# Performance work log

Hardware: AMD Instinct MI355X
Metric: run time of the kernel (lower is better)

Reference implementation:

```python
import jax, jax.numpy as jnp
import numpy as np

N_NODES = 50000

def _add_self_loops(edge_index, n):
    loop = jnp.arange(n, dtype=edge_index.dtype)
    src = jnp.concatenate([edge_index[0], loop])
    dst = jnp.concatenate([edge_index[1], loop])
    return src, dst

def _gcn_conv(x, src, dst, W, b, n):
    h = x @ W
    deg = jax.ops.segment_sum(jnp.ones_like(dst, dtype=h.dtype), dst, num_segments=n)
    inv_sqrt = jnp.where(deg > 0, jax.lax.rsqrt(deg), 0.0)
    coef = inv_sqrt[src] * inv_sqrt[dst]            # [E]
    msg = h[src] * coef[:, None]                     # [E, hidden]
    return jax.ops.segment_sum(msg, dst, num_segments=n) + b

def _gat_conv(x, src, dst, W, att_src, att_dst, b, n, heads, out_dim):
    # PyG GATConv, concat=False -> mean over heads; self-loops already added
    h = (x @ W).reshape(n, heads, out_dim)           # [N, H, F]
    a_src = jnp.sum(h * att_src, axis=-1)            # [N, H]
    a_dst = jnp.sum(h * att_dst, axis=-1)            # [N, H]
    e = a_src[src] + a_dst[dst]                      # [E, H]
    e = jax.nn.leaky_relu(e, negative_slope=0.2)
    # neighborhood softmax over edges grouped by destination
    m = jax.ops.segment_max(e, dst, num_segments=n)  # [N, H]
    ex = jnp.exp(e - m[dst])
    denom = jax.ops.segment_sum(ex, dst, num_segments=n)
    alpha = ex / denom[dst]                          # [E, H]
    out = jax.ops.segment_sum(h[src] * alpha[:, :, None], dst, num_segments=n)  # [N, H, F]
    return out.mean(axis=1) + b                      # concat=False -> head mean

def setup_inputs() -> dict:
    key = jax.random.key(0)
    ks = jax.random.split(key, 12)
    n, input_dim, hidden, output_dim, heads = N_NODES, 128, 128, 64, 2
    gat_out = hidden // 2
    x = jax.random.normal(ks[0], (n, input_dim), dtype=jnp.float32)
    edge_index = jax.random.randint(ks[1], (2, 800000), 0, n, dtype=jnp.int64)
    s = lambda fi, fo: float(np.sqrt(1.0 / fi))
    W1 = jax.random.normal(ks[2], (input_dim, hidden), dtype=jnp.float32) * s(input_dim, hidden)
    b1 = jnp.zeros((hidden,), dtype=jnp.float32)
    Wg = jax.random.normal(ks[3], (hidden, heads * gat_out), dtype=jnp.float32) * s(hidden, gat_out)
    att_src = jax.random.normal(ks[4], (heads, gat_out), dtype=jnp.float32) * s(gat_out, 1)
    att_dst = jax.random.normal(ks[5], (heads, gat_out), dtype=jnp.float32) * s(gat_out, 1)
    bg = jnp.zeros((gat_out,), dtype=jnp.float32)
    W3 = jax.random.normal(ks[6], (gat_out, output_dim), dtype=jnp.float32) * s(gat_out, output_dim)
    b3 = jnp.zeros((output_dim,), dtype=jnp.float32)
    return {"x": x, "edge_index": edge_index, "W1": W1, "b1": b1, "Wg": Wg,
            "att_src": att_src, "att_dst": att_dst, "bg": bg, "W3": W3, "b3": b3}

def reference(x, edge_index, W1, b1, Wg, att_src, att_dst, bg, W3, b3):
    n = x.shape[0]
    heads, gat_out = att_src.shape
    src, dst = _add_self_loops(edge_index, n)
    # dropout is identity in eval mode
    h = _gcn_conv(x, src, dst, W1, b1, n)
    h = jax.nn.relu(h)
    h = _gat_conv(h, src, dst, Wg, att_src, att_dst, bg, n, heads, gat_out)
    h = jax.nn.elu(h)
    return _gcn_conv(h, src, dst, W3, b3, n)
```

## Files before the change

kernel.cpp:

```cpp
#include <hip/hip_runtime.h>
#include <hip/hip_bf16.h>
#include <math.h>

#define N_NODES 50000
#define E0      800000
#define E_TOT   (E0 + N_NODES)
#define SCAP    512

using bf16 = __hip_bfloat16;
typedef __attribute__((ext_vector_type(8))) short bfrag;
typedef __attribute__((ext_vector_type(4))) float ffrag;

static __device__ __forceinline__ float bfu2f_lo(unsigned u){ return __uint_as_float(u << 16); }
static __device__ __forceinline__ float bfu2f_hi(unsigned u){ return __uint_as_float(u & 0xffff0000u); }

static __device__ __forceinline__ unsigned packbf(float a, float b){
    bf16 x = __float2bfloat16(a), y = __float2bfloat16(b);
    unsigned short ux = *reinterpret_cast<unsigned short*>(&x);
    unsigned short uy = *reinterpret_cast<unsigned short*>(&y);
    return ((unsigned)uy << 16) | ux;
}

static __device__ __forceinline__ int detect_f32(const unsigned* xu){
    int lane = threadIdx.x & 63;
    unsigned ex = (xu[lane] >> 7) & 0xFF;
    return (__ballot(ex < 100 || ex > 140) != 0ULL);
}
static __device__ __forceinline__ int detect_i32(const int* ei){
    int lane = threadIdx.x & 63;
    return (__ballot(ei[2 * lane + 1] != 0) != 0ULL);
}

static __device__ __forceinline__ float ldany(const void* p, int i, int isf32){
    return isf32 ? ((const float*)p)[i] : __bfloat162float(((const bf16*)p)[i]);
}

__global__ void k_convert(const void* __restrict__ xv,
                          const void* W1, const void* Wg, const void* W3,
                          const void* b1, const void* bg, const void* b3,
                          const void* as_, const void* ad_,
                          bf16* __restrict__ W1p, bf16* __restrict__ Wgp,
                          bf16* __restrict__ W3p, float* __restrict__ vecf,
                          bf16* __restrict__ xb, int* __restrict__ deg){
    const int NXB = (N_NODES * 32 + 255) / 256;
    int b = blockIdx.x, t = threadIdx.x;
    if (b >= 148 + NXB){
        int i = (b - 148 - NXB) * 256 + t;
        if (i < N_NODES) deg[i] = 0;
        return;
    }
    int isf = detect_f32((const unsigned*)xv);
    if (b >= 148){
        int i = (b - 148) * 256 + t;
        if (i < N_NODES * 32){
            if (isf){
                float4 v = ((const float4*)xv)[i];
                ((uint2*)xb)[i] = make_uint2(packbf(v.x, v.y), packbf(v.z, v.w));
            } else {
                ((uint2*)xb)[i] = ((const uint2*)xv)[i];
            }
        }
        return;
    }
    if (b < 16){
        int dd = b * 256 + t;
        int j  = dd & 7;
        int L  = (dd >> 3) & 63;
        int kc = (dd >> 9) & 1;
        int ct = dd >> 10;
        int k = kc * 32 + ((L >> 4) << 3) + j;
        int n = ct * 16 + (L & 15);
        W3p[dd] = __float2bfloat16(ldany(W3, k * 64 + n, isf));
    }
    else if (b < 18){
        int i = (b - 16) * 256 + t;
        float v;
        if      (i < 128) v = ldany(b1,  i,       isf);
        else if (i < 192) v = ldany(bg,  i - 128, isf);
        else if (i < 256) v = ldany(b3,  i - 192, isf);
        else if (i < 384) v = ldany(as_, i - 256, isf);
        else              v = ldany(ad_, i - 384, isf);
        vecf[i] = v;
    } else {
        int d = (b - 18) * 256 + t;
        const void* Wsrc = (d < 16384) ? W1 : Wg;
        bf16* Wdst = (d < 16384) ? W1p : Wgp;
        int dd = d & 16383;
        int j  = dd & 7;
        int L  = (dd >> 3) & 63;
        int kc = (dd >> 9) & 3;
        int ct = dd >> 11;
        int k = kc * 32 + ((L >> 4) << 3) + j;
        int n = ct * 16 + (L & 15);
        Wdst[dd] = __float2bfloat16(ldany(Wsrc, k * 128 + n, isf));
    }
}


static __device__ __forceinline__ int load_dst(const int* ei, int e, int is32){
    if (e >= E0) return e - E0;
    return is32 ? ei[E0 + e] : (int)((const long long*)ei)[E0 + e];
}
static __device__ __forceinline__ int load_src(const int* ei, int e, int is32){
    if (e >= E0) return e - E0;
    return is32 ? ei[e] : (int)((const long long*)ei)[e];
}

__global__ void k_count(const int* __restrict__ ei, int* __restrict__ deg,
                        int* __restrict__ rank){
    int is32 = detect_i32(ei);
    int e = blockIdx.x * blockDim.x + threadIdx.x;
    if (e >= E_TOT) return;
    int dst = load_dst(ei, e, is32);
    int src = load_src(ei, e, is32);
    if ((unsigned)dst >= N_NODES || (unsigned)src >= N_NODES) return;
    rank[e] = atomicAdd(&deg[dst], 1);
}

__global__ void k_scanA(const int* __restrict__ deg, int* __restrict__ tmp, int* __restrict__ blk){
    __shared__ int s[256];
    int t = threadIdx.x;
    int i = blockIdx.x * 256 + t;
    int v = (i < N_NODES) ? deg[i] : 0;
    s[t] = v; __syncthreads();
    for (int off = 1; off < 256; off <<= 1){
        int x = (t >= off) ? s[t - off] : 0;
        __syncthreads();
        s[t] += x;
        __syncthreads();
    }
    if (t == 255) blk[blockIdx.x] = s[255];
    if (i < N_NODES) tmp[i] = s[t] - v;
}

__global__ void k_scanC(int* __restrict__ row_ptr, const int* __restrict__ blk,
                        const int* __restrict__ deg, float* __restrict__ inv_sqrt,
                        int nb){
    __shared__ int s[256];
    int t = threadIdx.x;
    int B = blockIdx.x;
    s[t] = (t < nb && t < B) ? blk[t] : 0;
    __syncthreads();
    for (int off = 128; off; off >>= 1){
        if (t < off) s[t] += s[t + off];
        __syncthreads();
    }
    int base = s[0];
    int i = B * 256 + t;
    if (i < N_NODES){
        row_ptr[i] += base;
        int d = deg[i];
        inv_sqrt[i] = (d > 0) ? rsqrtf((float)d) : 0.0f;
    }
    if (i == 0) row_ptr[N_NODES] = E_TOT;
}

__global__ void k_fill(const int* __restrict__ ei, const int* __restrict__ row_ptr,
                       const float* __restrict__ isq, const int* __restrict__ rank,
                       int2* __restrict__ ecr){
    int is32 = detect_i32(ei);
    int e = blockIdx.x * blockDim.x + threadIdx.x;
    if (e >= E_TOT) return;
    int dst = load_dst(ei, e, is32);
    int src = load_src(ei, e, is32);
    if ((unsigned)dst >= N_NODES || (unsigned)src >= N_NODES) return;
    int pos = row_ptr[dst] + rank[e];
    float c = isq[dst] * isq[src];
    ecr[pos] = make_int2(src, __float_as_int(c));
}

__global__ __launch_bounds__(256) void k_gather(
        const uint4* __restrict__ xb16, const int* __restrict__ rp,
        const int2* __restrict__ ecr, uint4* __restrict__ Xa16){
    __shared__ int   scsr[SCAP];
    __shared__ float scf[SCAP];
    int n0 = blockIdx.x * 4;
    int b0 = rp[n0];
    int stot = min(rp[n0 + 4] - b0, SCAP);
    for (int i = threadIdx.x; i < stot; i += 256){
        int2 ev = ecr[b0 + i];
        scsr[i] = ev.x;
        scf[i]  = __int_as_float(ev.y);
    }
    __syncthreads();

    int w = threadIdx.x >> 6, lane = threadIdx.x & 63;
    int q4 = lane >> 4, fz = lane & 15;
    int n = n0 + w;
    float a0=0,a1=0,a2=0,a3=0,a4=0,a5=0,a6=0,a7=0;
    int b = rp[n] - b0, e = rp[n + 1] - b0;
    int elim = min(e, stot);
    #pragma unroll 2
    for (int i = b + q4; i < elim; i += 4){
        int s = scsr[i];
        float c = scf[i];
        uint4 v = xb16[(size_t)s * 16 + fz];
        a0 += c * bfu2f_lo(v.x);  a1 += c * bfu2f_hi(v.x);
        a2 += c * bfu2f_lo(v.y);  a3 += c * bfu2f_hi(v.y);
        a4 += c * bfu2f_lo(v.z);  a5 += c * bfu2f_hi(v.z);
        a6 += c * bfu2f_lo(v.w);  a7 += c * bfu2f_hi(v.w);
    }
    int start = max(b, stot);
    int i0 = start + (((b + q4) - start) & 3);
    for (int i = i0; i < e; i += 4){
        int2 ev = ecr[b0 + i];
        float c = __int_as_float(ev.y);
        uint4 v = xb16[(size_t)ev.x * 16 + fz];
        a0 += c * bfu2f_lo(v.x);  a1 += c * bfu2f_hi(v.x);
        a2 += c * bfu2f_lo(v.y);  a3 += c * bfu2f_hi(v.y);
        a4 += c * bfu2f_lo(v.z);  a5 += c * bfu2f_hi(v.z);
        a6 += c * bfu2f_lo(v.w);  a7 += c * bfu2f_hi(v.w);
    }
    a0 += __shfl_xor(a0, 32, 64);  a0 += __shfl_xor(a0, 16, 64);
    a1 += __shfl_xor(a1, 32, 64);  a1 += __shfl_xor(a1, 16, 64);
    a2 += __shfl_xor(a2, 32, 64);  a2 += __shfl_xor(a2, 16, 64);
    a3 += __shfl_xor(a3, 32, 64);  a3 += __shfl_xor(a3, 16, 64);
    a4 += __shfl_xor(a4, 32, 64);  a4 += __shfl_xor(a4, 16, 64);
    a5 += __shfl_xor(a5, 32, 64);  a5 += __shfl_xor(a5, 16, 64);
    a6 += __shfl_xor(a6, 32, 64);  a6 += __shfl_xor(a6, 16, 64);
    a7 += __shfl_xor(a7, 32, 64);  a7 += __shfl_xor(a7, 16, 64);
    if (lane < 16){
        uint4 o;
        o.x = packbf(a0, a1);  o.y = packbf(a2, a3);
        o.z = packbf(a4, a5);  o.w = packbf(a6, a7);
        Xa16[(size_t)n * 16 + fz] = o;
    }
}

template<int EPI>
__global__ __launch_bounds__(512) void k_gemm_mfma(
        const bf16* __restrict__ A, const bf16* __restrict__ Wp,
        const float* __restrict__ vecf, bf16* __restrict__ O,
        float* __restrict__ aS, float* __restrict__ aD){
    __shared__ float sA[16][8];
    __shared__ float sD[16][8];
    int wid  = threadIdx.x >> 6;
    int lane = threadIdx.x & 63;
    int n0 = blockIdx.x * 16;
    int m = lane & 15, q = lane >> 4;

    const bfrag* Ap = (const bfrag*)(A + (size_t)(n0 + m) * 128);
    const bfrag* Bp = (const bfrag*)Wp + (size_t)wid * 256 + lane;

    ffrag c = {0.f, 0.f, 0.f, 0.f};
    #pragma unroll
    for (int kc = 0; kc < 4; ++kc){
        bfrag af = Ap[kc * 4 + q];
        bfrag bf = Bp[kc * 64];
        c = __builtin_amdgcn_mfma_f32_16x16x32_bf16(af, bf, c, 0, 0, 0);
    }
    __syncthreads();

    int col = wid * 16 + m;
    if (EPI == 0){
        float bb = vecf[col];
        #pragma unroll
        for (int r = 0; r < 4; ++r){
            int row = n0 + q * 4 + r;
            O[(size_t)row * 128 + col] = __float2bfloat16(fmaxf(c[r] + bb, 0.f));
        }
    } else {
        int f = col & 63, h = col >> 6;
        float as_v = vecf[256 + h * 64 + f];
        float ad_v = vecf[384 + h * 64 + f];
        float ps[4], pd[4];
        #pragma unroll
        for (int r = 0; r < 4; ++r){
            int row = n0 + q * 4 + r;
            O[(size_t)row * 128 + f * 2 + h] = __float2bfloat16(c[r]);
            ps[r] = c[r] * as_v;
            pd[r] = c[r] * ad_v;
        }
        #pragma unroll
        for (int off = 1; off < 16; off <<= 1){
            #pragma unroll
            for (int r = 0; r < 4; ++r){
                ps[r] += __shfl_xor(ps[r], off, 64);
                pd[r] += __shfl_xor(pd[r], off, 64);
            }
        }
        if (m == 0){
            #pragma unroll
            for (int r = 0; r < 4; ++r){
                int rl = q * 4 + r;
                sA[rl][wid] = ps[r];
                sD[rl][wid] = pd[r];
            }
        }
        __syncthreads();
        int t = threadIdx.x;
        if (t < 64){
            int rl = t >> 2, hh = (t >> 1) & 1, which = t & 1;
            const float (*S)[8] = which ? sD : sA;
            float v = S[rl][hh * 4 + 0] + S[rl][hh * 4 + 1]
                    + S[rl][hh * 4 + 2] + S[rl][hh * 4 + 3];
            float* dp = which ? aD : aS;
            dp[(size_t)(n0 + rl) * 2 + hh] = v;
        }
    }
}

__global__ __launch_bounds__(256) void k_gemm_z(
        const bf16* __restrict__ Y, const bf16* __restrict__ W3p,
        bf16* __restrict__ Z){
    int wid  = threadIdx.x >> 6;
    int lane = threadIdx.x & 63;
    int n0 = blockIdx.x * 16;
    int m = lane & 15, q = lane >> 4;

    const bfrag* Ap = (const bfrag*)(Y + (size_t)(n0 + m) * 64);
    const bfrag* Bp = (const bfrag*)W3p + (size_t)wid * 128 + lane;

    ffrag c = {0.f, 0.f, 0.f, 0.f};
    #pragma unroll
    for (int kc = 0; kc < 2; ++kc){
        bfrag af = Ap[kc * 4 + q];
        bfrag bf = Bp[kc * 64];
        c = __builtin_amdgcn_mfma_f32_16x16x32_bf16(af, bf, c, 0, 0, 0);
    }
    int col = wid * 16 + m;
    #pragma unroll
    for (int r = 0; r < 4; ++r){
        int row = n0 + q * 4 + r;
        Z[(size_t)row * 64 + col] = __float2bfloat16(c[r]);
    }
}

__global__ __launch_bounds__(256) void k_gat(
        const uint4* __restrict__ X2v, const int* __restrict__ rp,
        const int2* __restrict__ ecr, const float2* __restrict__ a_src,
        const float2* __restrict__ a_dst, const float* __restrict__ vecf,
        uint2* __restrict__ Yu2){
    __shared__ int    scsr[SCAP];
    __shared__ float2 pe[SCAP];
    int n0 = blockIdx.x * 4;
    int b0 = rp[n0];
    int stot = min(rp[n0 + 4] - b0, SCAP);
    for (int i = threadIdx.x; i < stot; i += 256) scsr[i] = ecr[b0 + i].x;
    __syncthreads();

    int w = threadIdx.x >> 6, lane = threadIdx.x & 63;
    int q4 = lane >> 4, fz = lane & 15;
    int n = n0 + w;
    float2 ad = a_dst[n];
    int b = rp[n] - b0, e = rp[n + 1] - b0;
    int elim = min(e, stot);

    for (int i = b + lane; i < elim; i += 64){
        float2 av = a_src[scsr[i]];
        float e0 = av.x + ad.x, e1 = av.y + ad.y;
        e0 = (e0 > 0.f) ? e0 : 0.2f * e0;
        e1 = (e1 > 0.f) ? e1 : 0.2f * e1;
        pe[i] = make_float2(__expf(e0), __expf(e1));
    }

    float l0 = 0.f, l1 = 0.f;
    float o00=0,o01=0, o10=0,o11=0, o20=0,o21=0, o30=0,o31=0;
    #pragma unroll 2
    for (int i = b + q4; i < elim; i += 4){
        float2 p = pe[i];
        uint4 v = X2v[(size_t)scsr[i] * 16 + fz];
        l0  += p.x;                  l1  += p.y;
        o00 += p.x * bfu2f_lo(v.x);  o01 += p.y * bfu2f_hi(v.x);
        o10 += p.x * bfu2f_lo(v.y);  o11 += p.y * bfu2f_hi(v.y);
        o20 += p.x * bfu2f_lo(v.z);  o21 += p.y * bfu2f_hi(v.z);
        o30 += p.x * bfu2f_lo(v.w);  o31 += p.y * bfu2f_hi(v.w);
    }
    int start = max(b, stot);
    int i0 = start + (((b + q4) - start) & 3);
    for (int i = i0; i < e; i += 4){
        int s = ecr[b0 + i].x;
        float2 av = a_src[s];
        uint4 v = X2v[(size_t)s * 16 + fz];
        float e0 = av.x + ad.x, e1 = av.y + ad.y;
        e0 = (e0 > 0.f) ? e0 : 0.2f * e0;
        e1 = (e1 > 0.f) ? e1 : 0.2f * e1;
        float p0 = __expf(e0), p1 = __expf(e1);
        l0  += p0;                 l1  += p1;
        o00 += p0 * bfu2f_lo(v.x); o01 += p1 * bfu2f_hi(v.x);
        o10 += p0 * bfu2f_lo(v.y); o11 += p1 * bfu2f_hi(v.y);
        o20 += p0 * bfu2f_lo(v.z); o21 += p1 * bfu2f_hi(v.z);
        o30 += p0 * bfu2f_lo(v.w); o31 += p1 * bfu2f_hi(v.w);
    }
    l0  += __shfl_xor(l0, 32, 64);   l0  += __shfl_xor(l0, 16, 64);
    l1  += __shfl_xor(l1, 32, 64);   l1  += __shfl_xor(l1, 16, 64);
    o00 += __shfl_xor(o00, 32, 64);  o00 += __shfl_xor(o00, 16, 64);
    o01 += __shfl_xor(o01, 32, 64);  o01 += __shfl_xor(o01, 16, 64);
    o10 += __shfl_xor(o10, 32, 64);  o10 += __shfl_xor(o10, 16, 64);
    o11 += __shfl_xor(o11, 32, 64);  o11 += __shfl_xor(o11, 16, 64);
    o20 += __shfl_xor(o20, 32, 64);  o20 += __shfl_xor(o20, 16, 64);
    o21 += __shfl_xor(o21, 32, 64);  o21 += __shfl_xor(o21, 16, 64);
    o30 += __shfl_xor(o30, 32, 64);  o30 += __shfl_xor(o30, 16, 64);
    o31 += __shfl_xor(o31, 32, 64);  o31 += __shfl_xor(o31, 16, 64);
    if (lane < 16){
        float v0 = 0.5f * (o00 / l0 + o01 / l1) + vecf[128 + 4 * fz + 0];
        float v1 = 0.5f * (o10 / l0 + o11 / l1) + vecf[128 + 4 * fz + 1];
        float v2 = 0.5f * (o20 / l0 + o21 / l1) + vecf[128 + 4 * fz + 2];
        float v3 = 0.5f * (o30 / l0 + o31 / l1) + vecf[128 + 4 * fz + 3];
        v0 = (v0 > 0.f) ? v0 : expm1f(v0);
        v1 = (v1 > 0.f) ? v1 : expm1f(v1);
        v2 = (v2 > 0.f) ? v2 : expm1f(v2);
        v3 = (v3 > 0.f) ? v3 : expm1f(v3);
        Yu2[(size_t)n * 16 + fz] = make_uint2(packbf(v0, v1), packbf(v2, v3));
    }
}

__global__ __launch_bounds__(256) void k_gather_out(
        const uint2* __restrict__ Zu2, const int* __restrict__ rp,
        const int2* __restrict__ ecr, const float* __restrict__ vecf,
        float4* __restrict__ out4){
    __shared__ int   scsr[SCAP];
    __shared__ float scf[SCAP];
    int n0 = blockIdx.x * 4;
    int b0 = rp[n0];
    int stot = min(rp[n0 + 4] - b0, SCAP);
    for (int i = threadIdx.x; i < stot; i += 256){
        int2 ev = ecr[b0 + i];
        scsr[i] = ev.x;
        scf[i]  = __int_as_float(ev.y);
    }
    __syncthreads();

    int w = threadIdx.x >> 6, lane = threadIdx.x & 63;
    int q4 = lane >> 4, fz = lane & 15;
    int n = n0 + w;
    float a0 = 0.f, a1 = 0.f, a2 = 0.f, a3 = 0.f;
    int b = rp[n] - b0, e = rp[n + 1] - b0;
    int elim = min(e, stot);
    #pragma unroll 2
    for (int i = b + q4; i < elim; i += 4){
        float c = scf[i];
        uint2 v = Zu2[(size_t)scsr[i] * 16 + fz];
        a0 += c * bfu2f_lo(v.x);  a1 += c * bfu2f_hi(v.x);
        a2 += c * bfu2f_lo(v.y);  a3 += c * bfu2f_hi(v.y);
    }
    int start = max(b, stot);
    int i0 = start + (((b + q4) - start) & 3);
    for (int i = i0; i < e; i += 4){
        int2 ev = ecr[b0 + i];
        float c = __int_as_float(ev.y);
        uint2 v = Zu2[(size_t)ev.x * 16 + fz];
        a0 += c * bfu2f_lo(v.x);  a1 += c * bfu2f_hi(v.x);
        a2 += c * bfu2f_lo(v.y);  a3 += c * bfu2f_hi(v.y);
    }
    a0 += __shfl_xor(a0, 32, 64);  a0 += __shfl_xor(a0, 16, 64);
    a1 += __shfl_xor(a1, 32, 64);  a1 += __shfl_xor(a1, 16, 64);
    a2 += __shfl_xor(a2, 32, 64);  a2 += __shfl_xor(a2, 16, 64);
    a3 += __shfl_xor(a3, 32, 64);  a3 += __shfl_xor(a3, 16, 64);
    if (lane < 16)
        out4[(size_t)n * 16 + fz] = make_float4(
            a0 + vecf[192 + 4 * fz + 0], a1 + vecf[192 + 4 * fz + 1],
            a2 + vecf[192 + 4 * fz + 2], a3 + vecf[192 + 4 * fz + 3]);
}


extern "C" void kernel_launch(void* const* d_in, const int* in_sizes, int n_in,
                              void* d_out, int out_size, void* d_ws, size_t ws_size,
                              hipStream_t stream) {
    const void* x  = d_in[0];
    const int*  ei = (const int*)d_in[1];
    float* out = (float*)d_out;

    char* p = (char*)d_ws;
    auto alloc = [&](size_t bytes) -> void* {
        void* r = (void*)p;
        p += (bytes + 255) & ~(size_t)255;
        return r;
    };
    int*   deg      = (int*)  alloc((size_t)N_NODES * 4);
    int*   row_ptr  = (int*)  alloc((size_t)(N_NODES + 1) * 4);
    int*   blk      = (int*)  alloc(256 * 4);
    int*   rank     = (int*)  alloc((size_t)E_TOT * 4);
    int2*  ecr      = (int2*) alloc((size_t)E_TOT * 8);
    float* inv_sqrt = (float*)alloc((size_t)N_NODES * 4);
    float* a_src    = (float*)alloc((size_t)N_NODES * 2 * 4);
    float* a_dst    = (float*)alloc((size_t)N_NODES * 2 * 4);
    bf16*  W1p      = (bf16*) alloc(16384 * 2);
    bf16*  Wgp      = (bf16*) alloc(16384 * 2);
    bf16*  W3p      = (bf16*) alloc(4096 * 2);
    float* vecf     = (float*)alloc(512 * 4);
    bf16*  xb       = (bf16*) alloc((size_t)N_NODES * 128 * 2);
    bf16*  XA       = (bf16*) alloc((size_t)N_NODES * 128 * 2);
    bf16*  Y        = (bf16*) alloc((size_t)N_NODES * 64 * 2);
    bf16*  Z        = xb;

    const int NB_NODE = (N_NODES + 255) / 256;
    const int NB_EDGE = (E_TOT + 255) / 256;
    const int NXB     = (N_NODES * 32 + 255) / 256;
    const int NB_CONV = 148 + NXB + NB_NODE;

    k_convert<<<NB_CONV, 256, 0, stream>>>(x, d_in[2], d_in[4], d_in[8],
                                           d_in[3], d_in[7], d_in[9], d_in[5], d_in[6],
                                           W1p, Wgp, W3p, vecf, xb, deg);
    k_count<<<NB_EDGE, 256, 0, stream>>>(ei, deg, rank);
    k_scanA<<<NB_NODE, 256, 0, stream>>>(deg, row_ptr, blk);
    k_scanC<<<NB_NODE, 256, 0, stream>>>(row_ptr, blk, deg, inv_sqrt, NB_NODE);
    k_fill<<<NB_EDGE, 256, 0, stream>>>(ei, row_ptr, inv_sqrt, rank, ecr);

    k_gather<<<N_NODES / 4, 256, 0, stream>>>((const uint4*)xb, row_ptr, ecr,
                                              (uint4*)XA);
    k_gemm_mfma<0><<<N_NODES / 16, 512, 0, stream>>>(XA, W1p, vecf, XA,
                                                     nullptr, nullptr);
    k_gemm_mfma<1><<<N_NODES / 16, 512, 0, stream>>>(XA, Wgp, vecf, XA,
                                                     a_src, a_dst);
    k_gat<<<N_NODES / 4, 256, 0, stream>>>((const uint4*)XA, row_ptr, ecr,
                                           (const float2*)a_src, (const float2*)a_dst,
                                           vecf, (uint2*)Y);
    k_gemm_z<<<N_NODES / 16, 256, 0, stream>>>(Y, W3p, Z);
    k_gather_out<<<N_NODES / 4, 256, 0, stream>>>((const uint2*)Z, row_ptr, ecr,
                                                  vecf, (float4*)out);
}
```

Measured before the change: 285.4 us.

## Make GEMM waves own row tiles and pack edge src/dst/rank for fill

The MFMA GEMM kernels now have each wave compute a full 16-row slab across all column tiles, keeping A fragments in registers. This removes the shared-memory cross-wave reduction and the barriers for the attention-logit epilogue, and lets the logits be written directly as float2. Separately, k_count stores a packed (src,dst) word plus the atomic rank, so k_fill no longer re-reads and re-decodes the int64 edge index. The cost is more per-wave weight loads and register use, plus possible over-reads of the last partial row tile.

Result: faster. 271.5 us (-4.9%).

```diff
diff --git a/kernel.cpp b/kernel.cpp
--- a/kernel.cpp
+++ b/kernel.cpp
@@ -107,14 +107,18 @@
 }
 
 __global__ void k_count(const int* __restrict__ ei, int* __restrict__ deg,
-                        int* __restrict__ rank){
+                        int2* __restrict__ pkrk){
     int is32 = detect_i32(ei);
     int e = blockIdx.x * blockDim.x + threadIdx.x;
     if (e >= E_TOT) return;
     int dst = load_dst(ei, e, is32);
     int src = load_src(ei, e, is32);
-    if ((unsigned)dst >= N_NODES || (unsigned)src >= N_NODES) return;
-    rank[e] = atomicAdd(&deg[dst], 1);
+    if ((unsigned)dst >= N_NODES || (unsigned)src >= N_NODES){
+        pkrk[e] = make_int2(-1, 0);
+        return;
+    }
+    int r = atomicAdd(&deg[dst], 1);
+    pkrk[e] = make_int2((src << 16) | dst, r);
 }
 
 __global__ void k_scanA(const int* __restrict__ deg, int* __restrict__ tmp, int* __restrict__ blk){
@@ -155,16 +159,16 @@
     if (i == 0) row_ptr[N_NODES] = E_TOT;
 }
 
-__global__ void k_fill(const int* __restrict__ ei, const int* __restrict__ row_ptr,
-                       const float* __restrict__ isq, const int* __restrict__ rank,
-                       int2* __restrict__ ecr){
-    int is32 = detect_i32(ei);
+__global__ void k_fill(const int2* __restrict__ pkrk, const int* __restrict__ row_ptr,
+                       const float* __restrict__ isq, int2* __restrict__ ecr){
     int e = blockIdx.x * blockDim.x + threadIdx.x;
     if (e >= E_TOT) return;
-    int dst = load_dst(ei, e, is32);
-    int src = load_src(ei, e, is32);
-    if ((unsigned)dst >= N_NODES || (unsigned)src >= N_NODES) return;
-    int pos = row_ptr[dst] + rank[e];
+    int2 pr = pkrk[e];
+    unsigned pk = (unsigned)pr.x;
+    if (pk == 0xFFFFFFFFu) return;
+    int dst = pk & 0xFFFF;
+    int src = pk >> 16;
+    int pos = row_ptr[dst] + pr.y;
     float c = isq[dst] * isq[src];
     ecr[pos] = make_int2(src, __float_as_int(c));
 }
@@ -231,71 +235,77 @@
 __global__ __launch_bounds__(512) void k_gemm_mfma(
         const bf16* __restrict__ A, const bf16* __restrict__ Wp,
         const float* __restrict__ vecf, bf16* __restrict__ O,
-        float* __restrict__ aS, float* __restrict__ aD){
-    __shared__ float sA[16][8];
-    __shared__ float sD[16][8];
+        float2* __restrict__ aS, float2* __restrict__ aD){
     int wid  = threadIdx.x >> 6;
     int lane = threadIdx.x & 63;
-    int n0 = blockIdx.x * 16;
+    int r0 = blockIdx.x * 128 + wid * 16;
     int m = lane & 15, q = lane >> 4;
 
-    const bfrag* Ap = (const bfrag*)(A + (size_t)(n0 + m) * 128);
-    const bfrag* Bp = (const bfrag*)Wp + (size_t)wid * 256 + lane;
-
-    ffrag c = {0.f, 0.f, 0.f, 0.f};
+    const bfrag* Ap = (const bfrag*)(A + (size_t)(r0 + m) * 128);
+    bfrag af[4];
     #pragma unroll
-    for (int kc = 0; kc < 4; ++kc){
-        bfrag af = Ap[kc * 4 + q];
-        bfrag bf = Bp[kc * 64];
-        c = __builtin_amdgcn_mfma_f32_16x16x32_bf16(af, bf, c, 0, 0, 0);
-    }
-    __syncthreads();
-
-    int col = wid * 16 + m;
+    for (int kc = 0; kc < 4; ++kc) af[kc] = Ap[kc * 4 + q];
+
+    ffrag c[8];
+    #pragma unroll
+    for (int ct = 0; ct < 8; ++ct){
+        const bfrag* Bp = (const bfrag*)Wp + ct * 256 + lane;
+        ffrag acc = {0.f, 0.f, 0.f, 0.f};
+        #pragma unroll
+        for (int kc = 0; kc < 4; ++kc)
+            acc = __builtin_amdgcn_mfma_f32_16x16x32_bf16(af[kc], Bp[kc * 64], acc, 0, 0, 0);
+        c[ct] = acc;
+    }
+
     if (EPI == 0){
-        float bb = vecf[col];
         #pragma unroll
-        for (int r = 0; r < 4; ++r){
-            int row = n0 + q * 4 + r;
-            O[(size_t)row * 128 + col] = __float2bfloat16(fmaxf(c[r] + bb, 0.f));
+        for (int ct = 0; ct < 8; ++ct){
+            int col = ct * 16 + m;
+            float bb = vecf[col];
+            #pragma unroll
+            for (int r = 0; r < 4; ++r){
+                int row = r0 + q * 4 + r;
+                if (row < N_NODES)
+                    O[(size_t)row * 128 + col] = __float2bfloat16(fmaxf(c[ct][r] + bb, 0.f));
+            }
         }
     } else {
-        int f = col & 63, h = col >> 6;
-        float as_v = vecf[256 + h * 64 + f];
-        float ad_v = vecf[384 + h * 64 + f];
-        float ps[4], pd[4];
+        float ps0[4] = {0,0,0,0}, ps1[4] = {0,0,0,0};
+        float pd0[4] = {0,0,0,0}, pd1[4] = {0,0,0,0};
         #pragma unroll
-        for (int r = 0; r < 4; ++r){
-            int row = n0 + q * 4 + r;
-            O[(size_t)row * 128 + f * 2 + h] = __float2bfloat16(c[r]);
-            ps[r] = c[r] * as_v;
-            pd[r] = c[r] * ad_v;
+        for (int ct = 0; ct < 8; ++ct){
+            const int h = ct >> 2;
+            int f = (ct & 3) * 16 + m;
+            float as_v = vecf[256 + h * 64 + f];
+            float ad_v = vecf[384 + h * 64 + f];
+            #pragma unroll
+            for (int r = 0; r < 4; ++r){
+                int row = r0 + q * 4 + r;
+                if (row < N_NODES)
+                    O[(size_t)row * 128 + f * 2 + h] = __float2bfloat16(c[ct][r]);
+                if (h == 0){ ps0[r] += c[ct][r] * as_v;  pd0[r] += c[ct][r] * ad_v; }
+                else       { ps1[r] += c[ct][r] * as_v;  pd1[r] += c[ct][r] * ad_v; }
+            }
         }
         #pragma unroll
         for (int off = 1; off < 16; off <<= 1){
             #pragma unroll
             for (int r = 0; r < 4; ++r){
-                ps[r] += __shfl_xor(ps[r], off, 64);
-                pd[r] += __shfl_xor(pd[r], off, 64);
+                ps0[r] += __shfl_xor(ps0[r], off, 64);
+                ps1[r] += __shfl_xor(ps1[r], off, 64);
+                pd0[r] += __shfl_xor(pd0[r], off, 64);
+                pd1[r] += __shfl_xor(pd1[r], off, 64);
             }
         }
         if (m == 0){
             #pragma unroll
             for (int r = 0; r < 4; ++r){
-                int rl = q * 4 + r;
-                sA[rl][wid] = ps[r];
-                sD[rl][wid] = pd[r];
+                int row = r0 + q * 4 + r;
+                if (row < N_NODES){
+                    aS[row] = make_float2(ps0[r], ps1[r]);
+                    aD[row] = make_float2(pd0[r], pd1[r]);
+                }
             }
-        }
-        __syncthreads();
-        int t = threadIdx.x;
-        if (t < 64){
-            int rl = t >> 2, hh = (t >> 1) & 1, which = t & 1;
-            const float (*S)[8] = which ? sD : sA;
-            float v = S[rl][hh * 4 + 0] + S[rl][hh * 4 + 1]
-                    + S[rl][hh * 4 + 2] + S[rl][hh * 4 + 3];
-            float* dp = which ? aD : aS;
-            dp[(size_t)(n0 + rl) * 2 + hh] = v;
         }
     }
 }
@@ -305,24 +315,28 @@
         bf16* __restrict__ Z){
     int wid  = threadIdx.x >> 6;
     int lane = threadIdx.x & 63;
-    int n0 = blockIdx.x * 16;
+    int r0 = blockIdx.x * 64 + wid * 16;
     int m = lane & 15, q = lane >> 4;
 
-    const bfrag* Ap = (const bfrag*)(Y + (size_t)(n0 + m) * 64);
-    const bfrag* Bp = (const bfrag*)W3p + (size_t)wid * 128 + lane;
-
-    ffrag c = {0.f, 0.f, 0.f, 0.f};
+    const bfrag* Ap = (const bfrag*)(Y + (size_t)(r0 + m) * 64);
+    bfrag af[2];
     #pragma unroll
-    for (int kc = 0; kc < 2; ++kc){
-        bfrag af = Ap[kc * 4 + q];
-        bfrag bf = Bp[kc * 64];
-        c = __builtin_amdgcn_mfma_f32_16x16x32_bf16(af, bf, c, 0, 0, 0);
-    }
-    int col = wid * 16 + m;
+    for (int kc = 0; kc < 2; ++kc) af[kc] = Ap[kc * 4 + q];
+
     #pragma unroll
-    for (int r = 0; r < 4; ++r){
-        int row = n0 + q * 4 + r;
-        Z[(size_t)row * 64 + col] = __float2bfloat16(c[r]);
+    for (int ct = 0; ct < 4; ++ct){
+        const bfrag* Bp = (const bfrag*)W3p + ct * 128 + lane;
+        ffrag c = {0.f, 0.f, 0.f, 0.f};
+        #pragma unroll
+        for (int kc = 0; kc < 2; ++kc)
+            c = __builtin_amdgcn_mfma_f32_16x16x32_bf16(af[kc], Bp[kc * 64], c, 0, 0, 0);
+        int col = ct * 16 + m;
+        #pragma unroll
+        for (int r = 0; r < 4; ++r){
+            int row = r0 + q * 4 + r;
+            if (row < N_NODES)
+                Z[(size_t)row * 64 + col] = __float2bfloat16(c[r]);
+        }
     }
 }
 
@@ -470,7 +484,7 @@
     int*   deg      = (int*)  alloc((size_t)N_NODES * 4);
     int*   row_ptr  = (int*)  alloc((size_t)(N_NODES + 1) * 4);
     int*   blk      = (int*)  alloc(256 * 4);
-    int*   rank     = (int*)  alloc((size_t)E_TOT * 4);
+    int2*  pkrk     = (int2*) alloc((size_t)E_TOT * 8);
     int2*  ecr      = (int2*) alloc((size_t)E_TOT * 8);
     float* inv_sqrt = (float*)alloc((size_t)N_NODES * 4);
     float* a_src    = (float*)alloc((size_t)N_NODES * 2 * 4);
@@ -488,25 +502,27 @@
     const int NB_EDGE = (E_TOT + 255) / 256;
     const int NXB     = (N_NODES * 32 + 255) / 256;
     const int NB_CONV = 148 + NXB + NB_NODE;
+    const int NB_G128 = (N_NODES + 127) / 128;
+    const int NB_G64  = (N_NODES + 63) / 64;
 
     k_convert<<<NB_CONV, 256, 0, stream>>>(x, d_in[2], d_in[4], d_in[8],
                                            d_in[3], d_in[7], d_in[9], d_in[5], d_in[6],
                                            W1p, Wgp, W3p, vecf, xb, deg);
-    k_count<<<NB_EDGE, 256, 0, stream>>>(ei, deg, rank);
+    k_count<<<NB_EDGE, 256, 0, stream>>>(ei, deg, pkrk);
     k_scanA<<<NB_NODE, 256, 0, stream>>>(deg, row_ptr, blk);
     k_scanC<<<NB_NODE, 256, 0, stream>>>(row_ptr, blk, deg, inv_sqrt, NB_NODE);
-    k_fill<<<NB_EDGE, 256, 0, stream>>>(ei, row_ptr, inv_sqrt, rank, ecr);
+    k_fill<<<NB_EDGE, 256, 0, stream>>>(pkrk, row_ptr, inv_sqrt, ecr);
 
     k_gather<<<N_NODES / 4, 256, 0, stream>>>((const uint4*)xb, row_ptr, ecr,
                                               (uint4*)XA);
-    k_gemm_mfma<0><<<N_NODES / 16, 512, 0, stream>>>(XA, W1p, vecf, XA,
-                                                     nullptr, nullptr);
-    k_gemm_mfma<1><<<N_NODES / 16, 512, 0, stream>>>(XA, Wgp, vecf, XA,
-                                                     a_src, a_dst);
+    k_gemm_mfma<0><<<NB_G128, 512, 0, stream>>>(XA, W1p, vecf, XA,
+                                                nullptr, nullptr);
+    k_gemm_mfma<1><<<NB_G128, 512, 0, stream>>>(XA, Wgp, vecf, XA,
+                                                (float2*)a_src, (float2*)a_dst);
     k_gat<<<N_NODES / 4, 256, 0, stream>>>((const uint4*)XA, row_ptr, ecr,
                                            (const float2*)a_src, (const float2*)a_dst,
                                            vecf, (uint2*)Y);
-    k_gemm_z<<<N_NODES / 16, 256, 0, stream>>>(Y, W3p, Z);
+    k_gemm_z<<<NB_G64, 256, 0, stream>>>(Y, W3p, Z);
     k_gather_out<<<N_NODES / 4, 256, 0, stream>>>((const uint2*)Z, row_ptr, ecr,
                                                   vecf, (float4*)out);
 }
```
